# Performance work log

Measured on AMD Instinct MI355X. Metric: run time of the kernel, lower is better.

Reference implementation:

```python
import jax, jax.numpy as jnp
import numpy as np

B, S, H, NH = 2, 2048, 1024, 16
HD = H // NH
R = 4
LORA_SCALE = 16.0 / 4.0  # lora_alpha / r


def lora_linear(x, W, b, A, Bm):
    # x: [b,t,in]; W: [out,in]; A: [r,in]; Bm: [out,r]
    base = jnp.einsum('bti,oi->bto', x, W) + b
    lora = jnp.einsum('btr,or->bto', jnp.einsum('bti,ri->btr', x, A), Bm)
    return base + LORA_SCALE * lora


def setup_inputs() -> dict:
    key = jax.random.key(0)
    ks = jax.random.split(key, 14)
    std = 1.0 / np.sqrt(H)
    d = {
        'hidden_states': jax.random.normal(ks[0], (B, S, H), dtype=jnp.float32),
        'attention_mask': jnp.zeros((B, 1, 1, S), dtype=jnp.float32),
    }
    for i, nm in enumerate(['q', 'k', 'v']):
        d[f'W{nm}'] = jax.random.normal(ks[1 + 4 * i], (H, H), dtype=jnp.float32) * std
        d[f'b{nm}'] = jnp.zeros((H,), dtype=jnp.float32)
        d[f'A{nm}'] = jax.random.normal(ks[2 + 4 * i], (R, H), dtype=jnp.float32) * std
        d[f'B{nm}'] = jnp.zeros((H, R), dtype=jnp.float32) + 0.01 * jax.random.normal(ks[3 + 4 * i], (H, R), dtype=jnp.float32)
    return d


def reference(hidden_states, attention_mask, Wq, bq, Aq, Bq, Wk, bk, Ak, Bk, Wv, bv, Av, Bv):
    def heads(p):  # [b,t,(h d)] -> [b,h,t,d]
        return p.reshape(B, S, NH, HD).transpose(0, 2, 1, 3)

    q = heads(lora_linear(hidden_states, Wq, bq, Aq, Bq))
    k = heads(lora_linear(hidden_states, Wk, bk, Ak, Bk))
    v = heads(lora_linear(hidden_states, Wv, bv, Av, Bv))

    scores = jnp.einsum('bhqd,bhkd->bhqk', q, k) / jnp.sqrt(jnp.float32(HD))
    causal = jnp.tril(jnp.ones((S, S), dtype=scores.dtype))
    causal = (1.0 - causal) * -10000.0  # [S,S], broadcast over b,h
    scores = scores + attention_mask + causal[None, None]
    weights = jax.nn.softmax(scores, axis=-1)  # dropout p=0 -> identity (eval)
    ctx = jnp.einsum('bhqk,bhkd->bhqd', weights, v)
    return ctx.transpose(0, 2, 1, 3).reshape(B, S, H)
```

## Files before the change

kernel.cpp:

```cpp
#include <hip/hip_runtime.h>
#include <stdint.h>

#define B_ 2
#define S_ 2048
#define H_ 1024
#define NH_ 16
#define HD_ 64
#define M_ 4096
#define LOG2E 1.44269504089f

typedef unsigned short u16;
typedef __bf16 bf16x8 __attribute__((ext_vector_type(8)));
typedef float  f32x4  __attribute__((ext_vector_type(4)));

#if __has_builtin(__builtin_amdgcn_exp2f)
#define EXP2(x) __builtin_amdgcn_exp2f(x)
#else
#define EXP2(x) exp2f(x)
#endif

#define WAITV4() asm volatile("s_waitcnt vmcnt(4)" ::: "memory")
#define WAITV0() asm volatile("s_waitcnt vmcnt(0)" ::: "memory")
#define LGKM0()  asm volatile("s_waitcnt lgkmcnt(0)" ::: "memory")
#define SCHED0() __builtin_amdgcn_sched_barrier(0)

__device__ inline u16 f2bf(float f) {
  union { float f; uint32_t u; } a; a.f = f;
  uint32_t r = a.u + 0x7FFFu + ((a.u >> 16) & 1u);
  return (u16)(r >> 16);
}

__device__ inline void gload_lds16(const void* g, void* l) {
  __builtin_amdgcn_global_load_lds((const __attribute__((address_space(1))) void*)g,
                                   (__attribute__((address_space(3))) void*)l, 16, 0, 0);
}

__global__ __launch_bounds__(256) void cvt_kernel(
    const float* __restrict__ x,
    const float* __restrict__ wq, const float* __restrict__ wk, const float* __restrict__ wv,
    const float* __restrict__ Aq, const float* __restrict__ Ak, const float* __restrict__ Av,
    const float* __restrict__ LBq, const float* __restrict__ LBk, const float* __restrict__ LBv,
    u16* __restrict__ xbf, u16* __restrict__ wbf) {
  const int XN = M_ * H_;
  const int WN = H_ * H_;
  int idx = (blockIdx.x * 256 + threadIdx.x) * 4;
  if (idx < XN) {
    float4 v = *(const float4*)(x + idx);
    *(ushort4*)(xbf + idx) = make_ushort4(f2bf(v.x), f2bf(v.y), f2bf(v.z), f2bf(v.w));
  } else {
    int j = idx - XN; int p = j >> 20; int off = j & (WN - 1);
    const float* W  = (p == 0) ? wq : (p == 1 ? wk : wv);
    const float* A  = (p == 0) ? Aq : (p == 1 ? Ak : Av);
    const float* LB = (p == 0) ? LBq : (p == 1 ? LBk : LBv);
    int n = off >> 10, k = off & 1023;
    float4 v  = *(const float4*)(W + off);
    f32x4 lb  = *(const f32x4*)&LB[n * 4];
    float4 a0 = *(const float4*)(A + k);
    float4 a1 = *(const float4*)(A + 1024 + k);
    float4 a2 = *(const float4*)(A + 2048 + k);
    float4 a3 = *(const float4*)(A + 3072 + k);
    v.x += 4.f * (lb.x * a0.x + lb.y * a1.x + lb.z * a2.x + lb.w * a3.x);
    v.y += 4.f * (lb.x * a0.y + lb.y * a1.y + lb.z * a2.y + lb.w * a3.y);
    v.z += 4.f * (lb.x * a0.z + lb.y * a1.z + lb.z * a2.z + lb.w * a3.z);
    v.w += 4.f * (lb.x * a0.w + lb.y * a1.w + lb.z * a2.w + lb.w * a3.w);
    *(ushort4*)(wbf + (p << 20) + off) = make_ushort4(f2bf(v.x), f2bf(v.y), f2bf(v.z), f2bf(v.w));
  }
}

template<int P>
__device__ __forceinline__ void gemm_body(
    const u16* __restrict__ xbf, const u16* __restrict__ wbf,
    const float* __restrict__ bias, u16* __restrict__ qkv,
    u16* __restrict__ As, u16* __restrict__ Bs) {
  const int n0 = blockIdx.x * 128;
  const int m0 = blockIdx.y * 128;
  const u16* Wp = wbf + (P << 20);
  const int tid = threadIdx.x, lane = tid & 63, w = tid >> 6;
  const int g = lane >> 4, q15 = lane & 15;
  const int wr = w >> 1, wc = w & 1;
  const f32x4 fzero = {0.f, 0.f, 0.f, 0.f};
  f32x4 acc[4][4];
#pragma unroll
  for (int mi = 0; mi < 4; ++mi)
#pragma unroll
    for (int ni = 0; ni < 4; ++ni) acc[mi][ni] = fzero;
  const int srow = lane >> 2;

  auto STAGE = [&](int buf, int k0) {
#pragma unroll
    for (int j = 0; j < 2; ++j) {
      int c = w * 2 + j;
      int row = c * 16 + srow;
      int uu = (lane & 3) ^ ((row >> 1) & 3);
      gload_lds16(xbf + (size_t)(m0 + row) * 1024 + k0 + uu * 8, As + buf * 4096 + c * 512);
      gload_lds16(Wp  + (size_t)(n0 + row) * 1024 + k0 + uu * 8, Bs + buf * 4096 + c * 512);
    }
  };

  STAGE(0, 0);
  STAGE(1, 32);
  int c0 = 0, c1 = 1, c2 = 2;
#pragma unroll 1
  for (int t = 0; t < 32; ++t) {
    if (t < 31) WAITV4(); else WAITV0();
    SCHED0();
    __builtin_amdgcn_s_barrier();
    if (t + 2 < 32) STAGE(c2, (t + 2) * 32);
    const u16* Ab = As + c0 * 4096;
    const u16* Bb = Bs + c0 * 4096;
    bf16x8 af[4], bfr[4];
#pragma unroll
    for (int mi = 0; mi < 4; ++mi) {
      int r = wr * 64 + mi * 16 + q15;
      af[mi] = *(const bf16x8*)&Ab[r * 32 + ((g ^ ((r >> 1) & 3)) * 8)];
    }
#pragma unroll
    for (int ni = 0; ni < 4; ++ni) {
      int r = wc * 64 + ni * 16 + q15;
      bfr[ni] = *(const bf16x8*)&Bb[r * 32 + ((g ^ ((r >> 1) & 3)) * 8)];
    }
    __builtin_amdgcn_s_setprio(1);
#pragma unroll
    for (int mi = 0; mi < 4; ++mi)
#pragma unroll
      for (int ni = 0; ni < 4; ++ni) {
        if (P == 2)
          acc[mi][ni] = __builtin_amdgcn_mfma_f32_16x16x32_bf16(af[mi], bfr[ni], acc[mi][ni], 0, 0, 0);
        else
          acc[mi][ni] = __builtin_amdgcn_mfma_f32_16x16x32_bf16(bfr[ni], af[mi], acc[mi][ni], 0, 0, 0);
      }
    __builtin_amdgcn_s_setprio(0);
    int tmp = c0; c0 = c1; c1 = c2; c2 = tmp;
  }

  if (P != 2) {
#pragma unroll
    for (int ni = 0; ni < 4; ++ni) {
      int nb = n0 + wc * 64 + ni * 16 + g * 4;
      f32x4 bi = *(const f32x4*)&bias[nb];
      int h = nb >> 6, dbase = nb & 63;
#pragma unroll
      for (int mi = 0; mi < 4; ++mi) {
        int m = m0 + wr * 64 + mi * 16 + q15;
        int bb = m >> 11, s = m & 2047;
        size_t bhs = (size_t)(bb * 16 + h) * 2048 + s;
        float v0 = acc[mi][ni][0] + bi.x, v1 = acc[mi][ni][1] + bi.y;
        float v2 = acc[mi][ni][2] + bi.z, v3 = acc[mi][ni][3] + bi.w;
        size_t addr;
        if (P == 0) {
          const float qs = 0.125f * LOG2E;
          v0 *= qs; v1 *= qs; v2 *= qs; v3 *= qs;
          addr = bhs * 64 + dbase;
        } else {
          int pos = (((dbase >> 3) ^ (s & 7)) << 3) | (dbase & 7);
          addr = 4194304 + bhs * 64 + pos;
        }
        *(ushort4*)&qkv[addr] = make_ushort4(f2bf(v0), f2bf(v1), f2bf(v2), f2bf(v3));
      }
    }
  } else {
    float biasv[4];
#pragma unroll
    for (int ni = 0; ni < 4; ++ni) biasv[ni] = bias[n0 + wc * 64 + ni * 16 + q15];
#pragma unroll
    for (int mi = 0; mi < 4; ++mi) {
      int mbase = m0 + wr * 64 + mi * 16 + g * 4;
      int bb = mbase >> 11, sbase = mbase & 2047;
      int sr = sbase & 31;
      int cba = (((sr >> 4) & 1) << 2) | (((sr >> 2) & 3) << 3);
      int sp = (sbase & 32) | cba;
#pragma unroll
      for (int ni = 0; ni < 4; ++ni) {
        int n = n0 + wc * 64 + ni * 16 + q15;
        int d = n & 63, h = n >> 6;
        int spp = (((sp >> 3) ^ (d & 7)) << 3) | (sp & 7);
        size_t addr = 8388608 + ((size_t)(bb * 16 + h) * 64 + d) * 2048 + (sbase & ~63) + spp;
        *(ushort4*)&qkv[addr] = make_ushort4(
            f2bf(acc[mi][ni][0] + biasv[ni]), f2bf(acc[mi][ni][1] + biasv[ni]),
            f2bf(acc[mi][ni][2] + biasv[ni]), f2bf(acc[mi][ni][3] + biasv[ni]));
      }
    }
  }
}

__global__ __launch_bounds__(256) void qkv_gemm(
    const u16* __restrict__ xbf, const u16* __restrict__ wbf,
    const float* __restrict__ bq, const float* __restrict__ bk, const float* __restrict__ bv,
    u16* __restrict__ qkv) {
  __shared__ __align__(16) u16 As[3 * 4096];
  __shared__ __align__(16) u16 Bs[3 * 4096];
  switch (blockIdx.z) {
    case 0: gemm_body<0>(xbf, wbf, bq, qkv, As, Bs); break;
    case 1: gemm_body<1>(xbf, wbf, bk, qkv, As, Bs); break;
    default: gemm_body<2>(xbf, wbf, bv, qkv, As, Bs); break;
  }
}

__global__ __launch_bounds__(256, 4) void attn_kernel(
    const u16* __restrict__ qkv, const float* __restrict__ amask, float* __restrict__ out) {
  const int bid = blockIdx.x;
  const int bh = (bid & 7) * 4 + ((bid >> 3) & 3);
  const int qt = 31 - (bid >> 5);
  const int b = bh >> 4, h = bh & 15;
  const int tid = threadIdx.x, lane = tid & 63, w = tid >> 6;
  const int g = lane >> 4, ql = lane & 15;
  const u16* Qb = qkv + (size_t)bh * 131072;
  const u16* Kb = qkv + 4194304 + (size_t)bh * 131072;
  const u16* Vb = qkv + 8388608 + (size_t)bh * 131072;
  __shared__ __align__(16) u16 Ks[2][64][64];
  __shared__ __align__(16) u16 Vs[2][64][64];
  __shared__ __align__(16) float MaskL[2048];
  const f32x4 fzero = {0.f, 0.f, 0.f, 0.f};

  {
    int o = tid * 4;
#pragma unroll
    for (int i = 0; i < 2; ++i) {
      float4 mv = *(const float4*)&amask[b * 2048 + o + i * 1024];
      mv.x *= LOG2E; mv.y *= LOG2E; mv.z *= LOG2E; mv.w *= LOG2E;
      *(float4*)&MaskL[o + i * 1024] = mv;
    }
  }
  LGKM0();
  SCHED0();

  auto STAGE = [&](int nb, int kb) {
#pragma unroll
    for (int j = 0; j < 2; ++j) {
      int rl = w * 16 + j * 8 + (lane >> 3);
      gload_lds16(Kb + (size_t)(kb + rl) * 64 + (lane & 7) * 8, &Ks[nb][w * 16 + j * 8][0]);
      gload_lds16(Vb + (size_t)rl * 2048 + kb + (lane & 7) * 8, &Vs[nb][w * 16 + j * 8][0]);
    }
  };

  const int qw = qt * 64 + w * 16;
  const int q  = qw + ql;
  bf16x8 qf[2];
#pragma unroll
  for (int ks = 0; ks < 2; ++ks)
    qf[ks] = *(const bf16x8*)&Qb[(size_t)q * 64 + ks * 32 + g * 8];
  f32x4 acc[4];
#pragma unroll
  for (int dt = 0; dt < 4; ++dt) acc[dt] = fzero;
  float mrun = -1e30f, lrun = 0.f;
  const int nt = qt + 1;

  STAGE(0, 0);
#pragma unroll 1
  for (int t = 0; t < nt; ++t) {
    WAITV0();
    SCHED0();
    __builtin_amdgcn_s_barrier();
    const int kb = t * 64;
    if (t + 1 < nt) STAGE((t + 1) & 1, kb + 64);
    const int cb = t & 1;
    f32x4 st[4];
#pragma unroll
    for (int k16 = 0; k16 < 4; ++k16) st[k16] = fzero;
    __builtin_amdgcn_s_setprio(1);
#pragma unroll
    for (int k16 = 0; k16 < 4; ++k16) {
      bf16x8 kf0 = *(const bf16x8*)&Ks[cb][k16 * 16 + ql][(g ^ (ql & 7)) * 8];
      bf16x8 kf1 = *(const bf16x8*)&Ks[cb][k16 * 16 + ql][((4 + g) ^ (ql & 7)) * 8];
      st[k16] = __builtin_amdgcn_mfma_f32_16x16x32_bf16(kf0, qf[0], st[k16], 0, 0, 0);
      st[k16] = __builtin_amdgcn_mfma_f32_16x16x32_bf16(kf1, qf[1], st[k16], 0, 0, 0);
    }
    __builtin_amdgcn_s_setprio(0);
    f32x4 mk[4];
#pragma unroll
    for (int k16 = 0; k16 < 4; ++k16) mk[k16] = *(const f32x4*)&MaskL[kb + k16 * 16 + g * 4];
    const bool needm = (t == nt - 1);
    float sc[16], pmax = -1e30f;
#pragma unroll
    for (int k16 = 0; k16 < 4; ++k16)
#pragma unroll
      for (int r = 0; r < 4; ++r) {
        float sv = st[k16][r] + mk[k16][r];
        if (needm) { int key = kb + k16 * 16 + g * 4 + r; sv = (key > q) ? -1e30f : sv; }
        sc[k16 * 4 + r] = sv;
        pmax = fmaxf(pmax, sv);
      }
    if (!__all(pmax <= mrun + 8.f)) {
      float pm = fmaxf(pmax, __shfl_xor(pmax, 16, 64));
      pm = fmaxf(pm, __shfl_xor(pm, 32, 64));
      const float mt = fmaxf(mrun, pm);
      const float scale = EXP2(mrun - mt);
      lrun *= scale;
#pragma unroll
      for (int dt = 0; dt < 4; ++dt) acc[dt] *= scale;
      mrun = mt;
    }
    float pv[16], ps = 0.f;
#pragma unroll
    for (int i = 0; i < 16; ++i) { pv[i] = EXP2(sc[i] - mrun); ps += pv[i]; }
    lrun += ps;
    bf16x8 pfv[2];
#pragma unroll
    for (int ksub = 0; ksub < 2; ++ksub)
#pragma unroll
      for (int j = 0; j < 4; ++j) {
        pfv[ksub][j]     = (__bf16)pv[ksub * 8 + j];
        pfv[ksub][4 + j] = (__bf16)pv[ksub * 8 + 4 + j];
      }
    __builtin_amdgcn_s_setprio(1);
#pragma unroll
    for (int dt = 0; dt < 4; ++dt)
#pragma unroll
      for (int ksub = 0; ksub < 2; ++ksub) {
        bf16x8 vf = *(const bf16x8*)&Vs[cb][dt * 16 + ql][((ksub * 4 + g) ^ (ql & 7)) * 8];
        acc[dt] = __builtin_amdgcn_mfma_f32_16x16x32_bf16(vf, pfv[ksub], acc[dt], 0, 0, 0);
      }
    __builtin_amdgcn_s_setprio(0);
  }

  float lsum = lrun;
  lsum += __shfl_xor(lsum, 16, 64);
  lsum += __shfl_xor(lsum, 32, 64);
  const float inv = 1.f / lsum;
#pragma unroll
  for (int dt = 0; dt < 4; ++dt) {
    f32x4 o = acc[dt] * inv;
    *(f32x4*)&out[((size_t)b * 2048 + q) * 1024 + h * 64 + dt * 16 + g * 4] = o;
  }
}

extern "C" void kernel_launch(void* const* d_in, const int* in_sizes, int n_in,
                              void* d_out, int out_size, void* d_ws, size_t ws_size,
                              hipStream_t stream) {
  const float* x  = (const float*)d_in[0];
  const float* am = (const float*)d_in[1];
  const float* Wq = (const float*)d_in[2];
  const float* bq = (const float*)d_in[3];
  const float* Aq = (const float*)d_in[4];
  const float* Bq = (const float*)d_in[5];
  const float* Wk = (const float*)d_in[6];
  const float* bk = (const float*)d_in[7];
  const float* Ak = (const float*)d_in[8];
  const float* Bk = (const float*)d_in[9];
  const float* Wv = (const float*)d_in[10];
  const float* bv = (const float*)d_in[11];
  const float* Av = (const float*)d_in[12];
  const float* Bv = (const float*)d_in[13];
  float* out = (float*)d_out;

  u16* xbf   = (u16*)d_ws;
  u16* wbf   = xbf + 4194304;
  u16* qkv   = wbf + 3145728;

  cvt_kernel<<<7168, 256, 0, stream>>>(x, Wq, Wk, Wv, Aq, Ak, Av, Bq, Bk, Bv, xbf, wbf);
  qkv_gemm<<<dim3(8, 32, 3), 256, 0, stream>>>(xbf, wbf, bq, bk, bv, qkv);
  attn_kernel<<<1024, 256, 0, stream>>>(qkv, am, out);
}
```

Measured before the change: 89.31 us.

## Process 128 queries per attention block, fold mask into MFMA accumulator init

Each wave in the attention kernel now handles two 16-row query groups, so a block covers 128 queries and the grid shrinks from 1024 to 512 blocks. Each K/V tile staged in LDS is therefore reused for twice as many queries. The log2e-scaled mask is precomputed in the conversion kernel and loaded per tile into registers (prefetched one tile ahead), where it seeds the QK MFMA accumulator in place of a separate add. This removes the per-block LDS mask fill, but it doubles register pressure (occupancy hint drops from 4 to 2), makes the causal tail coarser, and leaves fewer blocks to balance load across the GPU.

```diff
diff --git a/kernel.cpp b/kernel.cpp
--- a/kernel.cpp
+++ b/kernel.cpp
@@ -21,7 +21,6 @@
 
 #define WAITV4() asm volatile("s_waitcnt vmcnt(4)" ::: "memory")
 #define WAITV0() asm volatile("s_waitcnt vmcnt(0)" ::: "memory")
-#define LGKM0()  asm volatile("s_waitcnt lgkmcnt(0)" ::: "memory")
 #define SCHED0() __builtin_amdgcn_sched_barrier(0)
 
 __device__ inline u16 f2bf(float f) {
@@ -40,14 +39,16 @@
     const float* __restrict__ wq, const float* __restrict__ wk, const float* __restrict__ wv,
     const float* __restrict__ Aq, const float* __restrict__ Ak, const float* __restrict__ Av,
     const float* __restrict__ LBq, const float* __restrict__ LBk, const float* __restrict__ LBv,
-    u16* __restrict__ xbf, u16* __restrict__ wbf) {
+    const float* __restrict__ amask,
+    u16* __restrict__ xbf, u16* __restrict__ wbf, float* __restrict__ maskl2e) {
   const int XN = M_ * H_;
   const int WN = H_ * H_;
+  const int total = XN + 3 * WN;
   int idx = (blockIdx.x * 256 + threadIdx.x) * 4;
   if (idx < XN) {
     float4 v = *(const float4*)(x + idx);
     *(ushort4*)(xbf + idx) = make_ushort4(f2bf(v.x), f2bf(v.y), f2bf(v.z), f2bf(v.w));
-  } else {
+  } else if (idx < total) {
     int j = idx - XN; int p = j >> 20; int off = j & (WN - 1);
     const float* W  = (p == 0) ? wq : (p == 1 ? wk : wv);
     const float* A  = (p == 0) ? Aq : (p == 1 ? Ak : Av);
@@ -64,6 +65,13 @@
     v.z += 4.f * (lb.x * a0.z + lb.y * a1.z + lb.z * a2.z + lb.w * a3.z);
     v.w += 4.f * (lb.x * a0.w + lb.y * a1.w + lb.z * a2.w + lb.w * a3.w);
     *(ushort4*)(wbf + (p << 20) + off) = make_ushort4(f2bf(v.x), f2bf(v.y), f2bf(v.z), f2bf(v.w));
+  } else {
+    int mi = idx - total;
+    if (mi < B_ * S_) {
+      float4 mv = *(const float4*)(amask + mi);
+      mv.x *= LOG2E; mv.y *= LOG2E; mv.z *= LOG2E; mv.w *= LOG2E;
+      *(float4*)(maskl2e + mi) = mv;
+    }
   }
 }
 
@@ -196,33 +204,20 @@
   }
 }
 
-__global__ __launch_bounds__(256, 4) void attn_kernel(
-    const u16* __restrict__ qkv, const float* __restrict__ amask, float* __restrict__ out) {
+__global__ __launch_bounds__(256, 2) void attn_kernel(
+    const u16* __restrict__ qkv, const float* __restrict__ maskl2e, float* __restrict__ out) {
   const int bid = blockIdx.x;
   const int bh = (bid & 7) * 4 + ((bid >> 3) & 3);
-  const int qt = 31 - (bid >> 5);
+  const int qt = 15 - (bid >> 5);
   const int b = bh >> 4, h = bh & 15;
   const int tid = threadIdx.x, lane = tid & 63, w = tid >> 6;
   const int g = lane >> 4, ql = lane & 15;
   const u16* Qb = qkv + (size_t)bh * 131072;
   const u16* Kb = qkv + 4194304 + (size_t)bh * 131072;
   const u16* Vb = qkv + 8388608 + (size_t)bh * 131072;
+  const float* Mb = maskl2e + b * 2048;
   __shared__ __align__(16) u16 Ks[2][64][64];
   __shared__ __align__(16) u16 Vs[2][64][64];
-  __shared__ __align__(16) float MaskL[2048];
-  const f32x4 fzero = {0.f, 0.f, 0.f, 0.f};
-
-  {
-    int o = tid * 4;
-#pragma unroll
-    for (int i = 0; i < 2; ++i) {
-      float4 mv = *(const float4*)&amask[b * 2048 + o + i * 1024];
-      mv.x *= LOG2E; mv.y *= LOG2E; mv.z *= LOG2E; mv.w *= LOG2E;
-      *(float4*)&MaskL[o + i * 1024] = mv;
-    }
-  }
-  LGKM0();
-  SCHED0();
 
   auto STAGE = [&](int nb, int kb) {
 #pragma unroll
@@ -233,94 +228,124 @@
     }
   };
 
-  const int qw = qt * 64 + w * 16;
-  const int q  = qw + ql;
-  bf16x8 qf[2];
-#pragma unroll
-  for (int ks = 0; ks < 2; ++ks)
-    qf[ks] = *(const bf16x8*)&Qb[(size_t)q * 64 + ks * 32 + g * 8];
-  f32x4 acc[4];
-#pragma unroll
-  for (int dt = 0; dt < 4; ++dt) acc[dt] = fzero;
-  float mrun = -1e30f, lrun = 0.f;
-  const int nt = qt + 1;
-
+  const int qbase = qt * 128 + w * 32;
+  bf16x8 qf[2][2];
+#pragma unroll
+  for (int qg = 0; qg < 2; ++qg)
+#pragma unroll
+    for (int ks = 0; ks < 2; ++ks)
+      qf[qg][ks] = *(const bf16x8*)&Qb[(size_t)(qbase + qg * 16 + ql) * 64 + ks * 32 + g * 8];
+  const f32x4 fzero = {0.f, 0.f, 0.f, 0.f};
+  f32x4 acc[2][4];
+#pragma unroll
+  for (int qg = 0; qg < 2; ++qg)
+#pragma unroll
+    for (int dt = 0; dt < 4; ++dt) acc[qg][dt] = fzero;
+  float mrun[2] = {-1e30f, -1e30f}, lrun[2] = {0.f, 0.f};
+  const int nt = 2 * qt + 2;
+
+  f32x4 mkC[4], mkN[4];
   STAGE(0, 0);
+#pragma unroll
+  for (int k16 = 0; k16 < 4; ++k16) mkC[k16] = *(const f32x4*)&Mb[k16 * 16 + g * 4];
+
 #pragma unroll 1
   for (int t = 0; t < nt; ++t) {
     WAITV0();
     SCHED0();
     __builtin_amdgcn_s_barrier();
     const int kb = t * 64;
-    if (t + 1 < nt) STAGE((t + 1) & 1, kb + 64);
+    if (t + 1 < nt) {
+      STAGE((t + 1) & 1, kb + 64);
+#pragma unroll
+      for (int k16 = 0; k16 < 4; ++k16) mkN[k16] = *(const f32x4*)&Mb[kb + 64 + k16 * 16 + g * 4];
+    }
     const int cb = t & 1;
-    f32x4 st[4];
-#pragma unroll
-    for (int k16 = 0; k16 < 4; ++k16) st[k16] = fzero;
+    f32x4 st[2][4];
     __builtin_amdgcn_s_setprio(1);
 #pragma unroll
     for (int k16 = 0; k16 < 4; ++k16) {
       bf16x8 kf0 = *(const bf16x8*)&Ks[cb][k16 * 16 + ql][(g ^ (ql & 7)) * 8];
       bf16x8 kf1 = *(const bf16x8*)&Ks[cb][k16 * 16 + ql][((4 + g) ^ (ql & 7)) * 8];
-      st[k16] = __builtin_amdgcn_mfma_f32_16x16x32_bf16(kf0, qf[0], st[k16], 0, 0, 0);
-      st[k16] = __builtin_amdgcn_mfma_f32_16x16x32_bf16(kf1, qf[1], st[k16], 0, 0, 0);
+      st[0][k16] = __builtin_amdgcn_mfma_f32_16x16x32_bf16(kf0, qf[0][0], mkC[k16], 0, 0, 0);
+      st[0][k16] = __builtin_amdgcn_mfma_f32_16x16x32_bf16(kf1, qf[0][1], st[0][k16], 0, 0, 0);
+      st[1][k16] = __builtin_amdgcn_mfma_f32_16x16x32_bf16(kf0, qf[1][0], mkC[k16], 0, 0, 0);
+      st[1][k16] = __builtin_amdgcn_mfma_f32_16x16x32_bf16(kf1, qf[1][1], st[1][k16], 0, 0, 0);
     }
     __builtin_amdgcn_s_setprio(0);
-    f32x4 mk[4];
-#pragma unroll
-    for (int k16 = 0; k16 < 4; ++k16) mk[k16] = *(const f32x4*)&MaskL[kb + k16 * 16 + g * 4];
-    const bool needm = (t == nt - 1);
-    float sc[16], pmax = -1e30f;
-#pragma unroll
-    for (int k16 = 0; k16 < 4; ++k16)
-#pragma unroll
-      for (int r = 0; r < 4; ++r) {
-        float sv = st[k16][r] + mk[k16][r];
-        if (needm) { int key = kb + k16 * 16 + g * 4 + r; sv = (key > q) ? -1e30f : sv; }
-        sc[k16 * 4 + r] = sv;
-        pmax = fmaxf(pmax, sv);
-      }
-    if (!__all(pmax <= mrun + 8.f)) {
-      float pm = fmaxf(pmax, __shfl_xor(pmax, 16, 64));
-      pm = fmaxf(pm, __shfl_xor(pm, 32, 64));
-      const float mt = fmaxf(mrun, pm);
-      const float scale = EXP2(mrun - mt);
-      lrun *= scale;
-#pragma unroll
-      for (int dt = 0; dt < 4; ++dt) acc[dt] *= scale;
-      mrun = mt;
-    }
-    float pv[16], ps = 0.f;
-#pragma unroll
-    for (int i = 0; i < 16; ++i) { pv[i] = EXP2(sc[i] - mrun); ps += pv[i]; }
-    lrun += ps;
-    bf16x8 pfv[2];
-#pragma unroll
-    for (int ksub = 0; ksub < 2; ++ksub)
-#pragma unroll
-      for (int j = 0; j < 4; ++j) {
-        pfv[ksub][j]     = (__bf16)pv[ksub * 8 + j];
-        pfv[ksub][4 + j] = (__bf16)pv[ksub * 8 + 4 + j];
-      }
+    bf16x8 pfv[2][2];
+#pragma unroll
+    for (int qg = 0; qg < 2; ++qg) {
+      const int qq = qbase + qg * 16 + ql;
+      const bool needm = (kb + 63 > qbase + qg * 16);
+      float sc[16];
+#pragma unroll
+      for (int k16 = 0; k16 < 4; ++k16)
+#pragma unroll
+        for (int r = 0; r < 4; ++r) {
+          float sv = st[qg][k16][r];
+          if (needm) { int key = kb + k16 * 16 + g * 4 + r; sv = (key > qq) ? -1e30f : sv; }
+          sc[k16 * 4 + r] = sv;
+        }
+      float m8[8], m4[4];
+#pragma unroll
+      for (int i = 0; i < 8; ++i) m8[i] = fmaxf(sc[i], sc[i + 8]);
+#pragma unroll
+      for (int i = 0; i < 4; ++i) m4[i] = fmaxf(m8[i], m8[i + 4]);
+      float pmax = fmaxf(fmaxf(m4[0], m4[1]), fmaxf(m4[2], m4[3]));
+      if (!__all(pmax <= mrun[qg] + 8.f)) {
+        float pm = fmaxf(pmax, __shfl_xor(pmax, 16, 64));
+        pm = fmaxf(pm, __shfl_xor(pm, 32, 64));
+        const float mt = fmaxf(mrun[qg], pm);
+        const float scale = EXP2(mrun[qg] - mt);
+        lrun[qg] *= scale;
+#pragma unroll
+        for (int dt = 0; dt < 4; ++dt) acc[qg][dt] *= scale;
+        mrun[qg] = mt;
+      }
+      float pv[16];
+#pragma unroll
+      for (int i = 0; i < 16; ++i) pv[i] = EXP2(sc[i] - mrun[qg]);
+      float s8[8], s4[4];
+#pragma unroll
+      for (int i = 0; i < 8; ++i) s8[i] = pv[i] + pv[i + 8];
+#pragma unroll
+      for (int i = 0; i < 4; ++i) s4[i] = s8[i] + s8[i + 4];
+      lrun[qg] += (s4[0] + s4[1]) + (s4[2] + s4[3]);
+#pragma unroll
+      for (int ksub = 0; ksub < 2; ++ksub)
+#pragma unroll
+        for (int j = 0; j < 4; ++j) {
+          pfv[qg][ksub][j]     = (__bf16)pv[ksub * 8 + j];
+          pfv[qg][ksub][4 + j] = (__bf16)pv[ksub * 8 + 4 + j];
+        }
+    }
     __builtin_amdgcn_s_setprio(1);
 #pragma unroll
     for (int dt = 0; dt < 4; ++dt)
 #pragma unroll
       for (int ksub = 0; ksub < 2; ++ksub) {
         bf16x8 vf = *(const bf16x8*)&Vs[cb][dt * 16 + ql][((ksub * 4 + g) ^ (ql & 7)) * 8];
-        acc[dt] = __builtin_amdgcn_mfma_f32_16x16x32_bf16(vf, pfv[ksub], acc[dt], 0, 0, 0);
+        acc[0][dt] = __builtin_amdgcn_mfma_f32_16x16x32_bf16(vf, pfv[0][ksub], acc[0][dt], 0, 0, 0);
+        acc[1][dt] = __builtin_amdgcn_mfma_f32_16x16x32_bf16(vf, pfv[1][ksub], acc[1][dt], 0, 0, 0);
       }
     __builtin_amdgcn_s_setprio(0);
-  }
-
-  float lsum = lrun;
-  lsum += __shfl_xor(lsum, 16, 64);
-  lsum += __shfl_xor(lsum, 32, 64);
-  const float inv = 1.f / lsum;
-#pragma unroll
-  for (int dt = 0; dt < 4; ++dt) {
-    f32x4 o = acc[dt] * inv;
-    *(f32x4*)&out[((size_t)b * 2048 + q) * 1024 + h * 64 + dt * 16 + g * 4] = o;
+#pragma unroll
+    for (int k16 = 0; k16 < 4; ++k16) mkC[k16] = mkN[k16];
+  }
+
+#pragma unroll
+  for (int qg = 0; qg < 2; ++qg) {
+    float lsum = lrun[qg];
+    lsum += __shfl_xor(lsum, 16, 64);
+    lsum += __shfl_xor(lsum, 32, 64);
+    const float inv = 1.f / lsum;
+    const int qq = qbase + qg * 16 + ql;
+#pragma unroll
+    for (int dt = 0; dt < 4; ++dt) {
+      f32x4 o = acc[qg][dt] * inv;
+      *(f32x4*)&out[((size_t)b * 2048 + qq) * 1024 + h * 64 + dt * 16 + g * 4] = o;
+    }
   }
 }
 
@@ -346,8 +371,9 @@
   u16* xbf   = (u16*)d_ws;
   u16* wbf   = xbf + 4194304;
   u16* qkv   = wbf + 3145728;
-
-  cvt_kernel<<<7168, 256, 0, stream>>>(x, Wq, Wk, Wv, Aq, Ak, Av, Bq, Bk, Bv, xbf, wbf);
+  float* mk  = (float*)(qkv + 12582912);
+
+  cvt_kernel<<<7172, 256, 0, stream>>>(x, Wq, Wk, Wv, Aq, Ak, Av, Bq, Bk, Bv, am, xbf, wbf, mk);
   qkv_gemm<<<dim3(8, 32, 3), 256, 0, stream>>>(xbf, wbf, bq, bk, bv, qkv);
-  attn_kernel<<<1024, 256, 0, stream>>>(qkv, am, out);
-}
+  attn_kernel<<<512, 256, 0, stream>>>(qkv, mk, out);
+}
```

New measurement: 106.1 us. 18.9% more time.

## Split KV range for long causal query tiles and merge partials in a new kernel

Applied to the files above, without the earlier changes.

Query tiles in the upper half of the causal sequence now have their key range split into two halves, each handled by a separate block. Each half writes a bf16 partial accumulator plus its running max and sum, and a new merge kernel combines the two. The goal is to shorten the longest block and balance work across CUs, at the cost of an extra launch, extra global traffic and bf16 rounding of the partials. The log2e mask scaling moves into the conversion kernel. The mask is now used as the initial MFMA accumulator and prefetched one tile ahead. The max and sum reductions become trees.

```diff
diff --git a/kernel.cpp b/kernel.cpp
--- a/kernel.cpp
+++ b/kernel.cpp
@@ -21,13 +21,15 @@
 
 #define WAITV4() asm volatile("s_waitcnt vmcnt(4)" ::: "memory")
 #define WAITV0() asm volatile("s_waitcnt vmcnt(0)" ::: "memory")
-#define LGKM0()  asm volatile("s_waitcnt lgkmcnt(0)" ::: "memory")
 #define SCHED0() __builtin_amdgcn_sched_barrier(0)
 
 __device__ inline u16 f2bf(float f) {
   union { float f; uint32_t u; } a; a.f = f;
   uint32_t r = a.u + 0x7FFFu + ((a.u >> 16) & 1u);
   return (u16)(r >> 16);
+}
+__device__ inline float bf2f(u16 v) {
+  union { uint32_t u; float f; } a; a.u = ((uint32_t)v) << 16; return a.f;
 }
 
 __device__ inline void gload_lds16(const void* g, void* l) {
@@ -40,14 +42,16 @@
     const float* __restrict__ wq, const float* __restrict__ wk, const float* __restrict__ wv,
     const float* __restrict__ Aq, const float* __restrict__ Ak, const float* __restrict__ Av,
     const float* __restrict__ LBq, const float* __restrict__ LBk, const float* __restrict__ LBv,
-    u16* __restrict__ xbf, u16* __restrict__ wbf) {
+    const float* __restrict__ amask,
+    u16* __restrict__ xbf, u16* __restrict__ wbf, float* __restrict__ maskl2e) {
   const int XN = M_ * H_;
   const int WN = H_ * H_;
+  const int total = XN + 3 * WN;
   int idx = (blockIdx.x * 256 + threadIdx.x) * 4;
   if (idx < XN) {
     float4 v = *(const float4*)(x + idx);
     *(ushort4*)(xbf + idx) = make_ushort4(f2bf(v.x), f2bf(v.y), f2bf(v.z), f2bf(v.w));
-  } else {
+  } else if (idx < total) {
     int j = idx - XN; int p = j >> 20; int off = j & (WN - 1);
     const float* W  = (p == 0) ? wq : (p == 1 ? wk : wv);
     const float* A  = (p == 0) ? Aq : (p == 1 ? Ak : Av);
@@ -64,6 +68,13 @@
     v.z += 4.f * (lb.x * a0.z + lb.y * a1.z + lb.z * a2.z + lb.w * a3.z);
     v.w += 4.f * (lb.x * a0.w + lb.y * a1.w + lb.z * a2.w + lb.w * a3.w);
     *(ushort4*)(wbf + (p << 20) + off) = make_ushort4(f2bf(v.x), f2bf(v.y), f2bf(v.z), f2bf(v.w));
+  } else {
+    int mi = idx - total;
+    if (mi < B_ * S_) {
+      float4 mv = *(const float4*)(amask + mi);
+      mv.x *= LOG2E; mv.y *= LOG2E; mv.z *= LOG2E; mv.w *= LOG2E;
+      *(float4*)(maskl2e + mi) = mv;
+    }
   }
 }
 
@@ -197,32 +208,40 @@
 }
 
 __global__ __launch_bounds__(256, 4) void attn_kernel(
-    const u16* __restrict__ qkv, const float* __restrict__ amask, float* __restrict__ out) {
+    const u16* __restrict__ qkv, const float* __restrict__ maskl2e, float* __restrict__ out,
+    u16* __restrict__ pacc, float* __restrict__ pml) {
   const int bid = blockIdx.x;
-  const int bh = (bid & 7) * 4 + ((bid >> 3) & 3);
-  const int qt = 31 - (bid >> 5);
+  int bh, qt, t0, t1, rrec = 0;
+  bool split;
+  if (bid < 1024) {
+    split = true;
+    int xcd = bid & 7, idx = bid >> 3;
+    bh = xcd * 4 + (idx & 3);
+    int rest = idx >> 2;
+    qt = 31 - (rest >> 1);
+    int sp = rest & 1;
+    int ntt = qt + 1;
+    int h1 = ntt >> 1;
+    t0 = sp ? h1 : 0;
+    t1 = sp ? ntt : h1;
+    rrec = (bh * 16 + (qt - 16)) * 2 + sp;
+  } else {
+    split = false;
+    int v = bid - 1024;
+    bh = (v & 7) * 4 + ((v >> 3) & 3);
+    qt = 15 - (v >> 5);
+    t0 = 0; t1 = qt + 1;
+  }
   const int b = bh >> 4, h = bh & 15;
   const int tid = threadIdx.x, lane = tid & 63, w = tid >> 6;
   const int g = lane >> 4, ql = lane & 15;
   const u16* Qb = qkv + (size_t)bh * 131072;
   const u16* Kb = qkv + 4194304 + (size_t)bh * 131072;
   const u16* Vb = qkv + 8388608 + (size_t)bh * 131072;
+  const float* Mb = maskl2e + b * 2048;
   __shared__ __align__(16) u16 Ks[2][64][64];
   __shared__ __align__(16) u16 Vs[2][64][64];
-  __shared__ __align__(16) float MaskL[2048];
   const f32x4 fzero = {0.f, 0.f, 0.f, 0.f};
-
-  {
-    int o = tid * 4;
-#pragma unroll
-    for (int i = 0; i < 2; ++i) {
-      float4 mv = *(const float4*)&amask[b * 2048 + o + i * 1024];
-      mv.x *= LOG2E; mv.y *= LOG2E; mv.z *= LOG2E; mv.w *= LOG2E;
-      *(float4*)&MaskL[o + i * 1024] = mv;
-    }
-  }
-  LGKM0();
-  SCHED0();
 
   auto STAGE = [&](int nb, int kb) {
 #pragma unroll
@@ -243,43 +262,52 @@
 #pragma unroll
   for (int dt = 0; dt < 4; ++dt) acc[dt] = fzero;
   float mrun = -1e30f, lrun = 0.f;
-  const int nt = qt + 1;
-
-  STAGE(0, 0);
+  const int nloc = t1 - t0;
+
+  f32x4 mkC[4], mkN[4];
+  STAGE(0, t0 * 64);
+#pragma unroll
+  for (int k16 = 0; k16 < 4; ++k16) mkC[k16] = *(const f32x4*)&Mb[t0 * 64 + k16 * 16 + g * 4];
+
 #pragma unroll 1
-  for (int t = 0; t < nt; ++t) {
+  for (int lt = 0; lt < nloc; ++lt) {
+    const int t = t0 + lt;
     WAITV0();
     SCHED0();
     __builtin_amdgcn_s_barrier();
     const int kb = t * 64;
-    if (t + 1 < nt) STAGE((t + 1) & 1, kb + 64);
-    const int cb = t & 1;
+    if (lt + 1 < nloc) {
+      STAGE((lt + 1) & 1, kb + 64);
+#pragma unroll
+      for (int k16 = 0; k16 < 4; ++k16) mkN[k16] = *(const f32x4*)&Mb[kb + 64 + k16 * 16 + g * 4];
+    }
+    const int cb = lt & 1;
     f32x4 st[4];
-#pragma unroll
-    for (int k16 = 0; k16 < 4; ++k16) st[k16] = fzero;
     __builtin_amdgcn_s_setprio(1);
 #pragma unroll
     for (int k16 = 0; k16 < 4; ++k16) {
       bf16x8 kf0 = *(const bf16x8*)&Ks[cb][k16 * 16 + ql][(g ^ (ql & 7)) * 8];
       bf16x8 kf1 = *(const bf16x8*)&Ks[cb][k16 * 16 + ql][((4 + g) ^ (ql & 7)) * 8];
-      st[k16] = __builtin_amdgcn_mfma_f32_16x16x32_bf16(kf0, qf[0], st[k16], 0, 0, 0);
+      st[k16] = __builtin_amdgcn_mfma_f32_16x16x32_bf16(kf0, qf[0], mkC[k16], 0, 0, 0);
       st[k16] = __builtin_amdgcn_mfma_f32_16x16x32_bf16(kf1, qf[1], st[k16], 0, 0, 0);
     }
     __builtin_amdgcn_s_setprio(0);
-    f32x4 mk[4];
-#pragma unroll
-    for (int k16 = 0; k16 < 4; ++k16) mk[k16] = *(const f32x4*)&MaskL[kb + k16 * 16 + g * 4];
-    const bool needm = (t == nt - 1);
-    float sc[16], pmax = -1e30f;
+    const bool needm = (t == qt);
+    float sc[16];
 #pragma unroll
     for (int k16 = 0; k16 < 4; ++k16)
 #pragma unroll
       for (int r = 0; r < 4; ++r) {
-        float sv = st[k16][r] + mk[k16][r];
+        float sv = st[k16][r];
         if (needm) { int key = kb + k16 * 16 + g * 4 + r; sv = (key > q) ? -1e30f : sv; }
         sc[k16 * 4 + r] = sv;
-        pmax = fmaxf(pmax, sv);
-      }
+      }
+    float m8[8], m4[4];
+#pragma unroll
+    for (int i = 0; i < 8; ++i) m8[i] = fmaxf(sc[i], sc[i + 8]);
+#pragma unroll
+    for (int i = 0; i < 4; ++i) m4[i] = fmaxf(m8[i], m8[i + 4]);
+    float pmax = fmaxf(fmaxf(m4[0], m4[1]), fmaxf(m4[2], m4[3]));
     if (!__all(pmax <= mrun + 8.f)) {
       float pm = fmaxf(pmax, __shfl_xor(pmax, 16, 64));
       pm = fmaxf(pm, __shfl_xor(pm, 32, 64));
@@ -290,10 +318,15 @@
       for (int dt = 0; dt < 4; ++dt) acc[dt] *= scale;
       mrun = mt;
     }
-    float pv[16], ps = 0.f;
-#pragma unroll
-    for (int i = 0; i < 16; ++i) { pv[i] = EXP2(sc[i] - mrun); ps += pv[i]; }
-    lrun += ps;
+    float pv[16];
+#pragma unroll
+    for (int i = 0; i < 16; ++i) pv[i] = EXP2(sc[i] - mrun);
+    float s8[8], s4[4];
+#pragma unroll
+    for (int i = 0; i < 8; ++i) s8[i] = pv[i] + pv[i + 8];
+#pragma unroll
+    for (int i = 0; i < 4; ++i) s4[i] = s8[i] + s8[i + 4];
+    lrun += (s4[0] + s4[1]) + (s4[2] + s4[3]);
     bf16x8 pfv[2];
 #pragma unroll
     for (int ksub = 0; ksub < 2; ++ksub)
@@ -311,16 +344,60 @@
         acc[dt] = __builtin_amdgcn_mfma_f32_16x16x32_bf16(vf, pfv[ksub], acc[dt], 0, 0, 0);
       }
     __builtin_amdgcn_s_setprio(0);
+#pragma unroll
+    for (int k16 = 0; k16 < 4; ++k16) mkC[k16] = mkN[k16];
   }
 
   float lsum = lrun;
   lsum += __shfl_xor(lsum, 16, 64);
   lsum += __shfl_xor(lsum, 32, 64);
-  const float inv = 1.f / lsum;
-#pragma unroll
-  for (int dt = 0; dt < 4; ++dt) {
-    f32x4 o = acc[dt] * inv;
-    *(f32x4*)&out[((size_t)b * 2048 + q) * 1024 + h * 64 + dt * 16 + g * 4] = o;
+  if (!split) {
+    const float inv = 1.f / lsum;
+#pragma unroll
+    for (int dt = 0; dt < 4; ++dt) {
+      f32x4 o = acc[dt] * inv;
+      *(f32x4*)&out[((size_t)b * 2048 + q) * 1024 + h * 64 + dt * 16 + g * 4] = o;
+    }
+  } else {
+    const int qloc = w * 16 + ql;
+#pragma unroll
+    for (int dt = 0; dt < 4; ++dt) {
+      *(ushort4*)&pacc[(size_t)rrec * 4096 + qloc * 64 + dt * 16 + g * 4] =
+          make_ushort4(f2bf(acc[dt][0]), f2bf(acc[dt][1]), f2bf(acc[dt][2]), f2bf(acc[dt][3]));
+    }
+    if (g == 0) {
+      pml[rrec * 128 + qloc] = mrun;
+      pml[rrec * 128 + 64 + qloc] = lsum;
+    }
+  }
+}
+
+__global__ __launch_bounds__(256) void merge_kernel(
+    const u16* __restrict__ pacc, const float* __restrict__ pml, float* __restrict__ out) {
+  const int mu = blockIdx.x;
+  const int bh = mu >> 4, qtm = (mu & 15) + 16;
+  const int b = bh >> 4, h = bh & 15;
+  const int r0 = mu * 2, r1 = r0 + 1;
+  const int tid = threadIdx.x;
+  const int ql = tid & 63, dc = (tid >> 6) * 16;
+  const float m0 = pml[r0 * 128 + ql], l0 = pml[r0 * 128 + 64 + ql];
+  const float m1 = pml[r1 * 128 + ql], l1 = pml[r1 * 128 + 64 + ql];
+  const float m  = fmaxf(m0, m1);
+  const float w0 = EXP2(m0 - m), w1 = EXP2(m1 - m);
+  const float inv = 1.f / (l0 * w0 + l1 * w1);
+  const u16* a0 = pacc + (size_t)r0 * 4096 + ql * 64 + dc;
+  const u16* a1 = pacc + (size_t)r1 * 4096 + ql * 64 + dc;
+  float* op = out + ((size_t)b * 2048 + qtm * 64 + ql) * 1024 + h * 64 + dc;
+#pragma unroll
+  for (int j = 0; j < 16; j += 4) {
+    ushort4 u0 = *(const ushort4*)(a0 + j);
+    ushort4 u1 = *(const ushort4*)(a1 + j);
+    f32x4 o;
+    o[0] = (bf2f(u0.x) * w0 + bf2f(u1.x) * w1) * inv;
+    o[1] = (bf2f(u0.y) * w0 + bf2f(u1.y) * w1) * inv;
+    o[2] = (bf2f(u0.z) * w0 + bf2f(u1.z) * w1) * inv;
+    o[3] = (bf2f(u0.w) * w0 + bf2f(u1.w) * w1) * inv;
+    *(f32x4*)(op + j) = o;
   }
 }
 
@@ -346,8 +423,12 @@
   u16* xbf   = (u16*)d_ws;
   u16* wbf   = xbf + 4194304;
   u16* qkv   = wbf + 3145728;
-
-  cvt_kernel<<<7168, 256, 0, stream>>>(x, Wq, Wk, Wv, Aq, Ak, Av, Bq, Bk, Bv, xbf, wbf);
+  float* mk  = (float*)(qkv + 12582912);
+  u16* pacc  = xbf;
+  float* pml = (float*)(xbf + 4194304);
+
+  cvt_kernel<<<7172, 256, 0, stream>>>(x, Wq, Wk, Wv, Aq, Ak, Av, Bq, Bk, Bv, am, xbf, wbf, mk);
   qkv_gemm<<<dim3(8, 32, 3), 256, 0, stream>>>(xbf, wbf, bq, bk, bv, qkv);
-  attn_kernel<<<1024, 256, 0, stream>>>(qkv, am, out);
-}
+  attn_kernel<<<1536, 256, 0, stream>>>(qkv, mk, out, pacc, pml);
+  merge_kernel<<<512, 256, 0, stream>>>(pacc, pml, out);
+}
```

After: 99.15 us. +11.0%, slower.
